# Optimization experiments

Measured on AMD Instinct MI355X. Metric: run time of the kernel, lower is better.

## Reference

```python
import jax, jax.numpy as jnp
import numpy as np

B, S, D, E = 8, 4096, 1024, 3
EPS = 1e-5


def setup_inputs() -> dict:
    key = jax.random.key(0)
    ks = jax.random.split(key, 4)
    s = 0.02  # init scale for weights
    return {
        "inputs": jax.random.normal(ks[0], (B, S, D), jnp.float32),
        "current_state": jnp.zeros((B, D), jnp.float32),
        "norm_w": jnp.ones((D,), jnp.float32),              # RMSNorm weight
        "router_w": jax.random.normal(ks[1], (D, E), jnp.float32) * s,
        "router_b": jnp.zeros((E,), jnp.float32),
        "w_gh": jax.random.normal(ks[2], (E, D, 2 * D), jnp.float32) * s,  # per-expert minGRU hidden+gate proj
        "w_out": jax.random.normal(ks[3], (E, D, D), jnp.float32) * s,     # per-expert proj_out
    }


def _rmsnorm(x, w, eps=EPS):
    return x * jax.lax.rsqrt(jnp.mean(x * x, axis=-1, keepdims=True) + eps) * w


def _g(x):
    # minGRU continuous activation g(x) = x + 0.5 for x >= 0 else sigmoid(x)
    return jnp.where(x >= 0, x + 0.5, jax.nn.sigmoid(x))


def reference(inputs, current_state, norm_w, router_w, router_b, w_gh, w_out):
    x = _rmsnorm(inputs, norm_w)                       # [B,S,D]
    # SMEAR: route per sample (mean-pooled features), soft-merge expert weights
    logits = jnp.mean(x, axis=1) @ router_w + router_b  # [B,E]
    probs = jax.nn.softmax(logits, axis=-1)             # [B,E]
    Wg = jnp.einsum('be,eij->bij', probs, w_gh)         # [B,D,2D] merged gate/hidden weights
    Wo = jnp.einsum('be,eij->bij', probs, w_out)        # [B,D,D]  merged output proj
    hg = jnp.einsum('bsi,bij->bsj', x, Wg)              # [B,S,2D]
    hid, gate = jnp.split(hg, 2, axis=-1)
    z = jax.nn.sigmoid(gate)                            # update gate
    a = 1.0 - z                                         # decay coefficient
    b = z * _g(hid)                                     # input term
    # fold initial state into first step: h_0 contribution
    b = b.at[:, 0].add(a[:, 0] * current_state)
    # linear recurrence h_t = a_t * h_{t-1} + b_t via associative scan over time
    def comb(c1, c2):
        a1, b1 = c1
        a2, b2 = c2
        return a1 * a2, a2 * b1 + b2
    _, h = jax.lax.associative_scan(comb, (a, b), axis=1)  # [B,S,D]
    new_state = h[:, -1]
    out = jnp.einsum('bsi,bij->bsj', h, Wo) + inputs       # proj_out + residual
    aux_loss = jnp.float32(0.0)
    return out, new_state, aux_loss
```

## Files before the change

kernel.cpp:

```cpp
#include <hip/hip_runtime.h>
#include <hip/hip_bf16.h>
#include <cstdint>
#include <cstddef>

using bf16 = __bf16;
typedef __bf16 bf16x8 __attribute__((ext_vector_type(8)));
typedef __bf16 bf16x4 __attribute__((ext_vector_type(4)));
typedef float  f32x4  __attribute__((ext_vector_type(4)));

#define DEV __device__ __forceinline__

DEV float sigmoidf_(float x) { return 1.0f / (1.0f + __expf(-x)); }

typedef __attribute__((address_space(1))) void as1_void;
typedef __attribute__((address_space(3))) void as3_void;

DEV void load16_lds(const void* g, void* l) {
  __builtin_amdgcn_global_load_lds((as1_void*)(void*)g, (as3_void*)l, 16, 0, 0);
}

__global__ __launch_bounds__(256) void k_rms_x(const float* __restrict__ inp,
                                               const float* __restrict__ nw,
                                               bf16* __restrict__ x) {
  const int row = blockIdx.x;
  const int t = threadIdx.x;
  const float* r = inp + (size_t)row * 1024 + t * 4;
  f32x4 v = *(const f32x4*)r;
  float ss = v[0]*v[0] + v[1]*v[1] + v[2]*v[2] + v[3]*v[3];
  __shared__ float red[4];
  for (int off = 32; off; off >>= 1) ss += __shfl_down(ss, off);
  if ((t & 63) == 0) red[t >> 6] = ss;
  __syncthreads();
  float tot = red[0] + red[1] + red[2] + red[3];
  float sc = rsqrtf(tot * (1.0f / 1024.0f) + 1e-5f);
  f32x4 w = *(const f32x4*)(nw + t * 4);
  bf16x4 o;
  o[0] = (bf16)(v[0] * sc * w[0]); o[1] = (bf16)(v[1] * sc * w[1]);
  o[2] = (bf16)(v[2] * sc * w[2]); o[3] = (bf16)(v[3] * sc * w[3]);
  *(bf16x4*)(x + (size_t)row * 1024 + t * 4) = o;
}

__global__ __launch_bounds__(256) void k_colsum(const bf16* __restrict__ x,
                                                float* __restrict__ part) {
  const int b = blockIdx.y, c = blockIdx.x;
  const int d = threadIdx.x * 4;
  f32x4 s = {0.f, 0.f, 0.f, 0.f};
  const bf16* base = x + ((size_t)b * 4096 + (size_t)c * 128) * 1024 + d;
  for (int i = 0; i < 128; ++i) {
    bf16x4 v = *(const bf16x4*)(base + (size_t)i * 1024);
    s[0] += (float)v[0]; s[1] += (float)v[1];
    s[2] += (float)v[2]; s[3] += (float)v[3];
  }
  *(f32x4*)(part + ((size_t)(b * 32 + c)) * 1024 + d) = s;
}

__global__ __launch_bounds__(256) void k_router(const float* __restrict__ part,
                                                const float* __restrict__ rw,
                                                const float* __restrict__ rb,
                                                float* __restrict__ probs,
                                                float* __restrict__ aux) {
  const int b = blockIdx.x;
  const int t = threadIdx.x;
  __shared__ float red[4];
  __shared__ float lg[3];
  f32x4 cs = {0.f, 0.f, 0.f, 0.f};
  #pragma unroll 8
  for (int c = 0; c < 32; ++c)
    cs += *(const f32x4*)(part + ((size_t)(b * 32 + c)) * 1024 + t * 4);
  for (int e = 0; e < 3; ++e) {
    float dot = cs[0] * rw[(t*4+0)*3+e] + cs[1] * rw[(t*4+1)*3+e]
              + cs[2] * rw[(t*4+2)*3+e] + cs[3] * rw[(t*4+3)*3+e];
    for (int off = 32; off; off >>= 1) dot += __shfl_down(dot, off);
    if ((t & 63) == 0) red[t >> 6] = dot;
    __syncthreads();
    if (t == 0) lg[e] = (red[0]+red[1]+red[2]+red[3]) * (1.0f/4096.0f) + rb[e];
    __syncthreads();
  }
  if (t == 0) {
    float m = fmaxf(lg[0], fmaxf(lg[1], lg[2]));
    float p0 = __expf(lg[0]-m), p1 = __expf(lg[1]-m), p2 = __expf(lg[2]-m);
    float inv = 1.0f / (p0 + p1 + p2);
    probs[b*3+0] = p0*inv; probs[b*3+1] = p1*inv; probs[b*3+2] = p2*inv;
    if (b == 0) *aux = 0.0f;
  }
}

__global__ __launch_bounds__(256) void k_mixT(const float* __restrict__ W,
                                              const float* __restrict__ probs,
                                              bf16* __restrict__ out,
                                              int Ncols) {
  const int b = blockIdx.z;
  const int i0 = blockIdx.y * 64;
  const int j0 = blockIdx.x * 64;
  const float p0 = probs[b*3+0], p1 = probs[b*3+1], p2 = probs[b*3+2];
  __shared__ float tile[64][68];
  const int t = threadIdx.x;
  const int jl = (t & 15) * 4;
  const size_t estr = (size_t)1024 * Ncols;
  for (int ii = 0; ii < 4; ++ii) {
    int il = (t >> 4) + ii * 16;
    const float* src = W + (size_t)(i0 + il) * Ncols + (j0 + jl);
    f32x4 v0 = *(const f32x4*)(src);
    f32x4 v1 = *(const f32x4*)(src + estr);
    f32x4 v2 = *(const f32x4*)(src + 2 * estr);
    f32x4 v = p0 * v0 + p1 * v1 + p2 * v2;
    tile[il][jl+0] = v[0]; tile[il][jl+1] = v[1];
    tile[il][jl+2] = v[2]; tile[il][jl+3] = v[3];
  }
  __syncthreads();
  bf16* ob = out + (size_t)b * Ncols * 1024;
  const int il2 = (t & 15) * 4;
  for (int jj = 0; jj < 4; ++jj) {
    int jl2 = (t >> 4) + jj * 16;
    bf16x4 o;
    o[0] = (bf16)tile[il2+0][jl2]; o[1] = (bf16)tile[il2+1][jl2];
    o[2] = (bf16)tile[il2+2][jl2]; o[3] = (bf16)tile[il2+3][jl2];
    *(bf16x4*)(ob + (size_t)(j0 + jl2) * 1024 + (i0 + il2)) = o;
  }
}

template<int EPI>
__global__ __launch_bounds__(512, 1) void k_gemm256(const bf16* __restrict__ A,
                                                    const bf16* __restrict__ Bt,
                                                    const float* __restrict__ addend,
                                                    float* __restrict__ Cout,
                                                    bf16* __restrict__ pa,
                                                    bf16* __restrict__ pb,
                                                    int M, int N, int K) {
  const int bz = blockIdx.z;
  const int nx = gridDim.x;
  const int nwg = nx * gridDim.y;
  const int orig = blockIdx.y * nx + blockIdx.x;
  const int swz = (orig & 7) * (nwg >> 3) + (orig >> 3);
  const int tm = swz / nx, tn = swz % nx;

  __shared__ __align__(16) char smem[131072];
  const int tid = threadIdx.x;
  const int lane = tid & 63, w = tid >> 6;
  const int l15 = lane & 15, quad = lane >> 4;
  const int wm = (w >> 2) * 128;
  const int wn = (w & 3) * 64;

  const bf16* Ab  = A  + (size_t)bz * M * K;
  const bf16* Btb = Bt + (size_t)bz * N * K;

  const int row0 = tid >> 3,          kc0 = (tid & 7) ^ (row0 & 7);
  const int row1 = (512 + tid) >> 3,  kc1 = (tid & 7) ^ (row1 & 7);

  auto browf = [&](int c) -> int {
    if constexpr (EPI == 0) {
      return tn * 128 + ((c >> 6) * 32) + (c & 31) + (((c & 63) >= 32) ? 1024 : 0);
    } else {
      return tn * 256 + c;
    }
  };
  const bf16* aS0_0 = Ab + (size_t)(tm*256 +       row0) * K + kc0 * 8;
  const bf16* aS0_1 = Ab + (size_t)(tm*256 +       row1) * K + kc1 * 8;
  const bf16* aS1_0 = Ab + (size_t)(tm*256 + 128 + row0) * K + kc0 * 8;
  const bf16* aS1_1 = Ab + (size_t)(tm*256 + 128 + row1) * K + kc1 * 8;
  const bf16* bS0_0 = Btb + (size_t)browf(row0)       * K + kc0 * 8;
  const bf16* bS0_1 = Btb + (size_t)browf(row1)       * K + kc1 * 8;
  const bf16* bS1_0 = Btb + (size_t)browf(128 + row0) * K + kc0 * 8;
  const bf16* bS1_1 = Btb + (size_t)browf(128 + row1) * K + kc1 * 8;

  const int ld0 = tid * 16;
  const int ld1 = 8192 + tid * 16;
  auto stage = [&](int buf, int u) {
    load16_lds(aS0_0 + u*64, smem + buf*32768 + ld0);
    load16_lds(aS0_1 + u*64, smem + buf*32768 + ld1);
    load16_lds(aS1_0 + u*64, smem + buf*32768 + 16384 + ld0);
    load16_lds(aS1_1 + u*64, smem + buf*32768 + 16384 + ld1);
    load16_lds(bS0_0 + u*64, smem + 65536 + buf*32768 + ld0);
    load16_lds(bS0_1 + u*64, smem + 65536 + buf*32768 + ld1);
    load16_lds(bS1_0 + u*64, smem + 65536 + buf*32768 + 16384 + ld0);
    load16_lds(bS1_1 + u*64, smem + 65536 + buf*32768 + 16384 + ld1);
  };

  f32x4 acc[8][4] = {};
  bf16x8 a[4][2], b0[2][2], b1[2][2];

  auto ldA = [&](int buf, int mq) {
    const bf16* base = (const bf16*)(smem + buf*32768);
    #pragma unroll
    for (int mi = 0; mi < 4; ++mi) {
      const int m = wm + mq*64 + mi*16 + l15;
      #pragma unroll
      for (int ks = 0; ks < 2; ++ks) {
        const int kc = ks*4 + quad;
        a[mi][ks] = *(const bf16x8*)(base + (size_t)(m*8 + (kc ^ (m & 7))) * 8);
      }
    }
  };
  auto ldB = [&](int buf, int nq, bf16x8 (&bb)[2][2]) {
    const bf16* base = (const bf16*)(smem + 65536 + buf*32768);
    #pragma unroll
    for (int ni = 0; ni < 2; ++ni) {
      const int n = wn + nq*32 + ni*16 + l15;
      #pragma unroll
      for (int ks = 0; ks < 2; ++ks) {
        const int kc = ks*4 + quad;
        bb[ni][ks] = *(const bf16x8*)(base + (size_t)(n*8 + (kc ^ (n & 7))) * 8);
      }
    }
  };

#define MMAC(MQ, NQ, BB)                                                        \
  _Pragma("unroll")                                                             \
  for (int mi = 0; mi < 4; ++mi) {                                              \
    _Pragma("unroll")                                                           \
    for (int ni = 0; ni < 2; ++ni) {                                            \
      f32x4 c_ = acc[(MQ)*4 + mi][(NQ)*2 + ni];                                 \
      c_ = __builtin_amdgcn_mfma_f32_16x16x32_bf16(a[mi][0], BB[ni][0], c_, 0, 0, 0); \
      c_ = __builtin_amdgcn_mfma_f32_16x16x32_bf16(a[mi][1], BB[ni][1], c_, 0, 0, 0); \
      acc[(MQ)*4 + mi][(NQ)*2 + ni] = c_;                                       \
    }                                                                           \
  }

  const int NT = K >> 6;

  stage(0, 0);
  __syncthreads();

  for (int t = 0; t < NT; ++t) {
    const int buf = t & 1;
    if (t + 1 < NT) stage(buf ^ 1, t + 1);
    ldA(buf, 0);
    ldB(buf, 0, b0);
    MMAC(0, 0, b0);
    ldB(buf, 1, b1);
    MMAC(0, 1, b1);
    ldA(buf, 1);
    MMAC(1, 1, b1);
    MMAC(1, 0, b0);
    __syncthreads();
  }

  if constexpr (EPI == 0) {
    bf16* Aab = pa + (size_t)bz * M * 1024;
    bf16* Bab = pb + (size_t)bz * M * 1024;
    const int jb = tn * 128 + (w & 3) * 32;
    const int rb = tm * 256 + wm;
    #pragma unroll
    for (int mi = 0; mi < 8; ++mi)
      #pragma unroll
      for (int ni = 0; ni < 2; ++ni)
        #pragma unroll
        for (int r = 0; r < 4; ++r) {
          const int srow = rb + mi * 16 + quad * 4 + r;
          float hid = acc[mi][ni][r];
          float gt  = acc[mi][ni + 2][r];
          float z = sigmoidf_(gt);
          float av = 1.0f - z;
          float gv = (hid >= 0.0f) ? (hid + 0.5f) : sigmoidf_(hid);
          float bv = z * gv;
          size_t oidx = (size_t)srow * 1024 + jb + ni * 16 + l15;
          Aab[oidx] = (bf16)av;
          Bab[oidx] = (bf16)bv;
        }
  } else {
    float* sC = (float*)smem;
    const int ST = 260;
    float* C = Cout + (size_t)bz * M * N;
    const float* Ain = addend + (size_t)bz * M * N;
    #pragma unroll
    for (int p = 0; p < 8; ++p) {
      if ((w >> 2) == (p >> 2)) {
        const int mi0 = (p & 3) * 2;
        #pragma unroll
        for (int mm = 0; mm < 2; ++mm)
          #pragma unroll
          for (int nt_ = 0; nt_ < 4; ++nt_)
            #pragma unroll
            for (int r = 0; r < 4; ++r) {
              const int rl = mm * 16 + quad * 4 + r;
              sC[rl * ST + (w & 3) * 64 + nt_ * 16 + l15] = acc[mi0 + mm][nt_][r];
            }
      }
      __syncthreads();
      #pragma unroll
      for (int i = 0; i < 4; ++i) {
        const int v = i * 512 + tid;
        const int rl = v >> 6, c4 = (v & 63) * 4;
        const int grow = tm * 256 + p * 32 + rl;
        const int gcol = tn * 256 + c4;
        f32x4 cv = *(f32x4*)(sC + rl * ST + c4);
        f32x4 ad = *(const f32x4*)(Ain + (size_t)grow * N + gcol);
        *(f32x4*)(C + (size_t)grow * N + gcol) = cv + ad;
      }
      __syncthreads();
    }
  }
#undef MMAC
}

__global__ __launch_bounds__(256) void k_scan1(const bf16* __restrict__ Aab,
                                               const bf16* __restrict__ Bab,
                                               float* __restrict__ cA,
                                               float* __restrict__ cB) {
  const int b = blockIdx.y, c = blockIdx.x;
  const int d = threadIdx.x * 4;
  f32x4 A = {1.f, 1.f, 1.f, 1.f}, Bv = {0.f, 0.f, 0.f, 0.f};
  const size_t base = ((size_t)(b * 4096 + c * 64)) * 1024 + d;
  #pragma unroll 4
  for (int i = 0; i < 64; ++i) {
    bf16x4 av = *(const bf16x4*)(Aab + base + (size_t)i * 1024);
    bf16x4 bv = *(const bf16x4*)(Bab + base + (size_t)i * 1024);
    #pragma unroll
    for (int j = 0; j < 4; ++j) {
      float a = (float)av[j], bb = (float)bv[j];
      A[j] *= a; Bv[j] = a * Bv[j] + bb;
    }
  }
  *(f32x4*)(cA + ((size_t)(b * 64 + c)) * 1024 + d) = A;
  *(f32x4*)(cB + ((size_t)(b * 64 + c)) * 1024 + d) = Bv;
}

__global__ __launch_bounds__(256) void k_scan2(const float* __restrict__ cA,
                                               const float* __restrict__ cB,
                                               const float* __restrict__ state,
                                               float* __restrict__ hin,
                                               float* __restrict__ ns) {
  const int gid = blockIdx.x * 256 + threadIdx.x;
  const int b = gid >> 10, d = gid & 1023;
  float h = state[gid];
  for (int c0 = 0; c0 < 64; c0 += 8) {
    float ar[8], br[8];
    #pragma unroll
    for (int i = 0; i < 8; ++i) {
      size_t idx = (((size_t)(b * 64 + c0 + i)) << 10) + d;
      ar[i] = cA[idx]; br[i] = cB[idx];
    }
    #pragma unroll
    for (int i = 0; i < 8; ++i) {
      size_t idx = (((size_t)(b * 64 + c0 + i)) << 10) + d;
      hin[idx] = h;
      h = ar[i] * h + br[i];
    }
  }
  ns[gid] = h;
}

__global__ __launch_bounds__(256) void k_scan3(const bf16* __restrict__ Aab,
                                               const bf16* __restrict__ Bab,
                                               const float* __restrict__ hin,
                                               bf16* __restrict__ hq) {
  const int b = blockIdx.y, c = blockIdx.x;
  const int d = threadIdx.x * 4;
  f32x4 h = *(const f32x4*)(hin + ((size_t)(b * 64 + c)) * 1024 + d);
  const size_t base = ((size_t)(b * 4096 + c * 64)) * 1024 + d;
  bf16* ob = hq + base;
  #pragma unroll 4
  for (int i = 0; i < 64; ++i) {
    bf16x4 av = *(const bf16x4*)(Aab + base + (size_t)i * 1024);
    bf16x4 bv = *(const bf16x4*)(Bab + base + (size_t)i * 1024);
    bf16x4 o;
    #pragma unroll
    for (int j = 0; j < 4; ++j) {
      h[j] = (float)av[j] * h[j] + (float)bv[j];
      o[j] = (bf16)h[j];
    }
    *(bf16x4*)(ob + (size_t)i * 1024) = o;
  }
}

extern "C" void kernel_launch(void* const* d_in, const int* in_sizes, int n_in,
                              void* d_out, int out_size, void* d_ws, size_t ws_size,
                              hipStream_t stream) {
  const float* inputs   = (const float*)d_in[0];
  const float* state    = (const float*)d_in[1];
  const float* norm_w   = (const float*)d_in[2];
  const float* router_w = (const float*)d_in[3];
  const float* router_b = (const float*)d_in[4];
  const float* w_gh     = (const float*)d_in[5];
  const float* w_out    = (const float*)d_in[6];

  float* out = (float*)d_out;
  float* new_state = out + (size_t)8 * 4096 * 1024;
  float* aux = new_state + 8 * 1024;

  char* ws = (char*)d_ws;
  size_t off = 0;
  auto alloc = [&](size_t bytes) {
    char* p = ws + off;
    off = (off + bytes + 255) & ~(size_t)255;
    return p;
  };
  bf16*  x    = (bf16*)alloc((size_t)8 * 4096 * 1024 * 2);
  bf16*  a_ar = (bf16*)alloc((size_t)8 * 4096 * 1024 * 2);
  bf16*  b_ar = (bf16*)alloc((size_t)8 * 4096 * 1024 * 2);
  bf16*  hq   = (bf16*)alloc((size_t)8 * 4096 * 1024 * 2);
  bf16*  WgT  = (bf16*)alloc((size_t)8 * 2048 * 1024 * 2);
  bf16*  WoT  = (bf16*)alloc((size_t)8 * 1024 * 1024 * 2);
  float* part = (float*)alloc((size_t)8 * 32 * 1024 * 4);
  float* probs = (float*)alloc(256);
  float* cA   = (float*)alloc((size_t)8 * 64 * 1024 * 4);
  float* cB   = (float*)alloc((size_t)8 * 64 * 1024 * 4);
  float* hin  = (float*)alloc((size_t)8 * 64 * 1024 * 4);
  (void)in_sizes; (void)n_in; (void)out_size; (void)ws_size;

  k_rms_x <<<32768, 256, 0, stream>>>(inputs, norm_w, x);
  k_colsum<<<dim3(32, 8), 256, 0, stream>>>(x, part);
  k_router<<<8, 256, 0, stream>>>(part, router_w, router_b, probs, aux);
  k_mixT  <<<dim3(32, 16, 8), 256, 0, stream>>>(w_gh, probs, WgT, 2048);
  k_mixT  <<<dim3(16, 16, 8), 256, 0, stream>>>(w_out, probs, WoT, 1024);
  k_gemm256<0><<<dim3(8, 16, 8), 512, 0, stream>>>(x, WgT, nullptr, nullptr,
                                                   a_ar, b_ar, 4096, 2048, 1024);
  k_scan1 <<<dim3(64, 8), 256, 0, stream>>>(a_ar, b_ar, cA, cB);
  k_scan2 <<<32, 256, 0, stream>>>(cA, cB, state, hin, new_state);
  k_scan3 <<<dim3(64, 8), 256, 0, stream>>>(a_ar, b_ar, hin, hq);
  k_gemm256<1><<<dim3(4, 16, 8), 512, 0, stream>>>(hq, WoT, inputs, out,
                                                   nullptr, nullptr, 4096, 1024, 1024);
}
```

Before: 580.1 us.

## Switch GEMM mainloop to 4-slot BK=32 pipeline with explicit vmcnt waits

Replaces the double-buffered BK=64 GEMM mainloop with a four-slot ring of BK=32 tiles kept three stages ahead. Each wait uses a fine-grained vmcnt count plus a raw s_barrier instead of a full __syncthreads, with a new paired-row swizzled LDS layout and precomputed fragment offsets. The aim is to hide global-to-LDS load latency better and cut sync cost. In exchange there are twice as many barriers per K, and the hand-counted vmcnt values and the slot reuse must be exactly right to avoid races.

```diff
diff --git a/kernel.cpp b/kernel.cpp
--- a/kernel.cpp
+++ b/kernel.cpp
@@ -18,6 +18,9 @@
 DEV void load16_lds(const void* g, void* l) {
   __builtin_amdgcn_global_load_lds((as1_void*)(void*)g, (as3_void*)l, 16, 0, 0);
 }
+
+#define SBAR()   __builtin_amdgcn_s_barrier()
+#define SCHED0() __builtin_amdgcn_sched_barrier(0)
 
 __global__ __launch_bounds__(256) void k_rms_x(const float* __restrict__ inp,
                                                const float* __restrict__ nw,
@@ -144,9 +147,6 @@
   const bf16* Ab  = A  + (size_t)bz * M * K;
   const bf16* Btb = Bt + (size_t)bz * N * K;
 
-  const int row0 = tid >> 3,          kc0 = (tid & 7) ^ (row0 & 7);
-  const int row1 = (512 + tid) >> 3,  kc1 = (tid & 7) ^ (row1 & 7);
-
   auto browf = [&](int c) -> int {
     if constexpr (EPI == 0) {
       return tn * 128 + ((c >> 6) * 32) + (c & 31) + (((c & 63) >= 32) ? 1024 : 0);
@@ -154,86 +154,76 @@
       return tn * 256 + c;
     }
   };
-  const bf16* aS0_0 = Ab + (size_t)(tm*256 +       row0) * K + kc0 * 8;
-  const bf16* aS0_1 = Ab + (size_t)(tm*256 +       row1) * K + kc1 * 8;
-  const bf16* aS1_0 = Ab + (size_t)(tm*256 + 128 + row0) * K + kc0 * 8;
-  const bf16* aS1_1 = Ab + (size_t)(tm*256 + 128 + row1) * K + kc1 * 8;
-  const bf16* bS0_0 = Btb + (size_t)browf(row0)       * K + kc0 * 8;
-  const bf16* bS0_1 = Btb + (size_t)browf(row1)       * K + kc1 * 8;
-  const bf16* bS1_0 = Btb + (size_t)browf(128 + row0) * K + kc0 * 8;
-  const bf16* bS1_1 = Btb + (size_t)browf(128 + row1) * K + kc1 * 8;
-
-  const int ld0 = tid * 16;
-  const int ld1 = 8192 + tid * 16;
-  auto stage = [&](int buf, int u) {
-    load16_lds(aS0_0 + u*64, smem + buf*32768 + ld0);
-    load16_lds(aS0_1 + u*64, smem + buf*32768 + ld1);
-    load16_lds(aS1_0 + u*64, smem + buf*32768 + 16384 + ld0);
-    load16_lds(aS1_1 + u*64, smem + buf*32768 + 16384 + ld1);
-    load16_lds(bS0_0 + u*64, smem + 65536 + buf*32768 + ld0);
-    load16_lds(bS0_1 + u*64, smem + 65536 + buf*32768 + ld1);
-    load16_lds(bS1_0 + u*64, smem + 65536 + buf*32768 + 16384 + ld0);
-    load16_lds(bS1_1 + u*64, smem + 65536 + buf*32768 + 16384 + ld1);
+
+  const int s7  = tid & 7;
+  const int r2a = tid >> 3;
+  const int g8v = s7 ^ (r2a & 7);
+  const int par = g8v >> 2;
+  const int gk  = g8v & 3;
+  const int rl0 = 2 * r2a + par;
+  const int rl1 = 128 + rl0;
+
+  const bf16* aSrc0 = Ab + (size_t)(tm*256 + rl0) * K + gk * 8;
+  const bf16* aSrc1 = Ab + (size_t)(tm*256 + rl1) * K + gk * 8;
+  const bf16* bSrc0 = Btb + (size_t)browf(rl0) * K + gk * 8;
+  const bf16* bSrc1 = Btb + (size_t)browf(rl1) * K + gk * 8;
+
+  auto stage = [&](int slot, int u) {
+    char* base = smem + slot * 32768;
+    load16_lds(aSrc0 + u*32, base + tid*16);
+    load16_lds(aSrc1 + u*32, base + 8192 + tid*16);
+    load16_lds(bSrc0 + u*32, base + 16384 + tid*16);
+    load16_lds(bSrc1 + u*32, base + 24576 + tid*16);
   };
 
+  int offA[8], offB[4];
+  #pragma unroll
+  for (int f = 0; f < 8; ++f) {
+    const int m = wm + (f >> 2) * 64 + (f & 3) * 16 + l15;
+    const int r2 = m >> 1;
+    offA[f] = r2 * 128 + (((((m & 1) << 2) | quad)) ^ (r2 & 7)) * 16;
+  }
+  #pragma unroll
+  for (int f = 0; f < 4; ++f) {
+    const int n = wn + (f >> 1) * 32 + (f & 1) * 16 + l15;
+    const int r2 = n >> 1;
+    offB[f] = r2 * 128 + (((((n & 1) << 2) | quad)) ^ (r2 & 7)) * 16;
+  }
+
   f32x4 acc[8][4] = {};
-  bf16x8 a[4][2], b0[2][2], b1[2][2];
-
-  auto ldA = [&](int buf, int mq) {
-    const bf16* base = (const bf16*)(smem + buf*32768);
-    #pragma unroll
-    for (int mi = 0; mi < 4; ++mi) {
-      const int m = wm + mq*64 + mi*16 + l15;
+  bf16x8 a[8], b[4];
+
+  const int NT = K >> 5;
+
+  stage(0, 0); stage(1, 1); stage(2, 2);
+  SCHED0();
+  asm volatile("s_waitcnt vmcnt(8)" ::: "memory");
+  SCHED0(); SBAR(); SCHED0();
+
+  for (int t = 0; t < NT; ++t) {
+    const int slot = t & 3;
+    if (t + 3 < NT) stage((t + 3) & 3, t + 3);
+    const char* ba = smem + slot * 32768;
+    const char* bbp = ba + 16384;
+    #pragma unroll
+    for (int f = 0; f < 8; ++f) a[f] = *(const bf16x8*)(ba + offA[f]);
+    #pragma unroll
+    for (int f = 0; f < 4; ++f) b[f] = *(const bf16x8*)(bbp + offB[f]);
+    #pragma unroll
+    for (int f = 0; f < 8; ++f)
       #pragma unroll
-      for (int ks = 0; ks < 2; ++ks) {
-        const int kc = ks*4 + quad;
-        a[mi][ks] = *(const bf16x8*)(base + (size_t)(m*8 + (kc ^ (m & 7))) * 8);
-      }
-    }
-  };
-  auto ldB = [&](int buf, int nq, bf16x8 (&bb)[2][2]) {
-    const bf16* base = (const bf16*)(smem + 65536 + buf*32768);
-    #pragma unroll
-    for (int ni = 0; ni < 2; ++ni) {
-      const int n = wn + nq*32 + ni*16 + l15;
-      #pragma unroll
-      for (int ks = 0; ks < 2; ++ks) {
-        const int kc = ks*4 + quad;
-        bb[ni][ks] = *(const bf16x8*)(base + (size_t)(n*8 + (kc ^ (n & 7))) * 8);
-      }
-    }
-  };
-
-#define MMAC(MQ, NQ, BB)                                                        \
-  _Pragma("unroll")                                                             \
-  for (int mi = 0; mi < 4; ++mi) {                                              \
-    _Pragma("unroll")                                                           \
-    for (int ni = 0; ni < 2; ++ni) {                                            \
-      f32x4 c_ = acc[(MQ)*4 + mi][(NQ)*2 + ni];                                 \
-      c_ = __builtin_amdgcn_mfma_f32_16x16x32_bf16(a[mi][0], BB[ni][0], c_, 0, 0, 0); \
-      c_ = __builtin_amdgcn_mfma_f32_16x16x32_bf16(a[mi][1], BB[ni][1], c_, 0, 0, 0); \
-      acc[(MQ)*4 + mi][(NQ)*2 + ni] = c_;                                       \
-    }                                                                           \
-  }
-
-  const int NT = K >> 6;
-
-  stage(0, 0);
+      for (int g = 0; g < 4; ++g)
+        acc[f][g] = __builtin_amdgcn_mfma_f32_16x16x32_bf16(a[f], b[g], acc[f][g], 0, 0, 0);
+    if (t + 1 < NT) {
+      SCHED0();
+      const int rem = NT - 2 - t;
+      if (rem >= 2)      { asm volatile("s_waitcnt vmcnt(8)" ::: "memory"); }
+      else if (rem == 1) { asm volatile("s_waitcnt vmcnt(4)" ::: "memory"); }
+      else               { asm volatile("s_waitcnt vmcnt(0)" ::: "memory"); }
+      SCHED0(); SBAR(); SCHED0();
+    }
+  }
   __syncthreads();
-
-  for (int t = 0; t < NT; ++t) {
-    const int buf = t & 1;
-    if (t + 1 < NT) stage(buf ^ 1, t + 1);
-    ldA(buf, 0);
-    ldB(buf, 0, b0);
-    MMAC(0, 0, b0);
-    ldB(buf, 1, b1);
-    MMAC(0, 1, b1);
-    ldA(buf, 1);
-    MMAC(1, 1, b1);
-    MMAC(1, 0, b0);
-    __syncthreads();
-  }
 
   if constexpr (EPI == 0) {
     bf16* Aab = pa + (size_t)bz * M * 1024;
@@ -290,7 +280,6 @@
       __syncthreads();
     }
   }
-#undef MMAC
 }
 
 __global__ __launch_bounds__(256) void k_scan1(const bf16* __restrict__ Aab,
```

Result: slower. 598.4 us (+3.1%).

## Restructure GEMM main loop into fine-grained half-tile prefetch pipeline with barriers and priorities

Applied to the files above, without the earlier changes.

Replaces the simple double-buffered GEMM loop with a schedule that splits each stage into A/B halves and issues global-to-LDS loads two iterations ahead, interleaved between MFMA quarter blocks. It uses explicit s_barrier, sched_barrier, manual vmcnt/lgkmcnt waits and s_setprio around MFMA clusters, with LDS offsets precomputed into registers. The aim is to hide global load latency and LDS reads behind matrix math. It adds more barriers per iteration and relies on hand-tuned wait counts, so the correctness of the buffer reuse timing is delicate.

```diff
diff --git a/kernel.cpp b/kernel.cpp
--- a/kernel.cpp
+++ b/kernel.cpp
@@ -18,6 +18,9 @@
 DEV void load16_lds(const void* g, void* l) {
   __builtin_amdgcn_global_load_lds((as1_void*)(void*)g, (as3_void*)l, 16, 0, 0);
 }
+
+#define SBAR()   __builtin_amdgcn_s_barrier()
+#define SCHED0() __builtin_amdgcn_sched_barrier(0)
 
 __global__ __launch_bounds__(256) void k_rms_x(const float* __restrict__ inp,
                                                const float* __restrict__ nw,
@@ -144,8 +147,8 @@
   const bf16* Ab  = A  + (size_t)bz * M * K;
   const bf16* Btb = Bt + (size_t)bz * N * K;
 
-  const int row0 = tid >> 3,          kc0 = (tid & 7) ^ (row0 & 7);
-  const int row1 = (512 + tid) >> 3,  kc1 = (tid & 7) ^ (row1 & 7);
+  const int rowh0 = tid >> 3,          kch0 = (tid & 7) ^ (rowh0 & 7);
+  const int rowh1 = (512 + tid) >> 3,  kch1 = (tid & 7) ^ (rowh1 & 7);
 
   auto browf = [&](int c) -> int {
     if constexpr (EPI == 0) {
@@ -154,86 +157,128 @@
       return tn * 256 + c;
     }
   };
-  const bf16* aS0_0 = Ab + (size_t)(tm*256 +       row0) * K + kc0 * 8;
-  const bf16* aS0_1 = Ab + (size_t)(tm*256 +       row1) * K + kc1 * 8;
-  const bf16* aS1_0 = Ab + (size_t)(tm*256 + 128 + row0) * K + kc0 * 8;
-  const bf16* aS1_1 = Ab + (size_t)(tm*256 + 128 + row1) * K + kc1 * 8;
-  const bf16* bS0_0 = Btb + (size_t)browf(row0)       * K + kc0 * 8;
-  const bf16* bS0_1 = Btb + (size_t)browf(row1)       * K + kc1 * 8;
-  const bf16* bS1_0 = Btb + (size_t)browf(128 + row0) * K + kc0 * 8;
-  const bf16* bS1_1 = Btb + (size_t)browf(128 + row1) * K + kc1 * 8;
-
-  const int ld0 = tid * 16;
-  const int ld1 = 8192 + tid * 16;
-  auto stage = [&](int buf, int u) {
-    load16_lds(aS0_0 + u*64, smem + buf*32768 + ld0);
-    load16_lds(aS0_1 + u*64, smem + buf*32768 + ld1);
-    load16_lds(aS1_0 + u*64, smem + buf*32768 + 16384 + ld0);
-    load16_lds(aS1_1 + u*64, smem + buf*32768 + 16384 + ld1);
-    load16_lds(bS0_0 + u*64, smem + 65536 + buf*32768 + ld0);
-    load16_lds(bS0_1 + u*64, smem + 65536 + buf*32768 + ld1);
-    load16_lds(bS1_0 + u*64, smem + 65536 + buf*32768 + 16384 + ld0);
-    load16_lds(bS1_1 + u*64, smem + 65536 + buf*32768 + 16384 + ld1);
+  const bf16* aS0_0 = Ab + (size_t)(tm*256 +       rowh0) * K + kch0 * 8;
+  const bf16* aS0_1 = Ab + (size_t)(tm*256 +       rowh1) * K + kch1 * 8;
+  const bf16* aS1_0 = Ab + (size_t)(tm*256 + 128 + rowh0) * K + kch0 * 8;
+  const bf16* aS1_1 = Ab + (size_t)(tm*256 + 128 + rowh1) * K + kch1 * 8;
+  const bf16* bS0_0 = Btb + (size_t)browf(rowh0)       * K + kch0 * 8;
+  const bf16* bS0_1 = Btb + (size_t)browf(rowh1)       * K + kch1 * 8;
+  const bf16* bS1_0 = Btb + (size_t)browf(128 + rowh0) * K + kch0 * 8;
+  const bf16* bS1_1 = Btb + (size_t)browf(128 + rowh1) * K + kch1 * 8;
+
+  auto stA = [&](int d, int h, int u) {
+    char* base = smem + (size_t)((d << 1) + h) * 16384;
+    load16_lds((h ? aS1_0 : aS0_0) + u * 64, base + tid * 16);
+    load16_lds((h ? aS1_1 : aS0_1) + u * 64, base + 8192 + tid * 16);
   };
-
-  f32x4 acc[8][4] = {};
-  bf16x8 a[4][2], b0[2][2], b1[2][2];
-
-  auto ldA = [&](int buf, int mq) {
-    const bf16* base = (const bf16*)(smem + buf*32768);
-    #pragma unroll
-    for (int mi = 0; mi < 4; ++mi) {
-      const int m = wm + mq*64 + mi*16 + l15;
+  auto stB = [&](int d, int h, int u) {
+    char* base = smem + 65536 + (size_t)((d << 1) + h) * 16384;
+    load16_lds((h ? bS1_0 : bS0_0) + u * 64, base + tid * 16);
+    load16_lds((h ? bS1_1 : bS0_1) + u * 64, base + 8192 + tid * 16);
+  };
+
+  const int ha = wm >> 7, hb = wn >> 7;
+  const int wnl = wn & 127;
+  int offA[2][4][2], offB[2][2][2];
+  #pragma unroll
+  for (int mq = 0; mq < 2; ++mq)
+    #pragma unroll
+    for (int mi = 0; mi < 4; ++mi)
       #pragma unroll
       for (int ks = 0; ks < 2; ++ks) {
-        const int kc = ks*4 + quad;
-        a[mi][ks] = *(const bf16x8*)(base + (size_t)(m*8 + (kc ^ (m & 7))) * 8);
+        const int mr = mq * 64 + mi * 16 + l15;
+        offA[mq][mi][ks] = mr * 128 + (((ks * 4 + quad)) ^ (mr & 7)) * 16;
       }
-    }
-  };
-  auto ldB = [&](int buf, int nq, bf16x8 (&bb)[2][2]) {
-    const bf16* base = (const bf16*)(smem + 65536 + buf*32768);
-    #pragma unroll
-    for (int ni = 0; ni < 2; ++ni) {
-      const int n = wn + nq*32 + ni*16 + l15;
+  #pragma unroll
+  for (int nq = 0; nq < 2; ++nq)
+    #pragma unroll
+    for (int ni = 0; ni < 2; ++ni)
       #pragma unroll
       for (int ks = 0; ks < 2; ++ks) {
-        const int kc = ks*4 + quad;
-        bb[ni][ks] = *(const bf16x8*)(base + (size_t)(n*8 + (kc ^ (n & 7))) * 8);
+        const int nr = wnl + nq * 32 + ni * 16 + l15;
+        offB[nq][ni][ks] = nr * 128 + (((ks * 4 + quad)) ^ (nr & 7)) * 16;
       }
-    }
-  };
-
-#define MMAC(MQ, NQ, BB)                                                        \
+
+  f32x4 acc[8][4] = {};
+  bf16x8 a0[4][2], a1[4][2], b0[2][2], b1[2][2];
+
+#define MMAC(MQ, NQ, AA, BB)                                                    \
   _Pragma("unroll")                                                             \
   for (int mi = 0; mi < 4; ++mi) {                                              \
     _Pragma("unroll")                                                           \
     for (int ni = 0; ni < 2; ++ni) {                                            \
       f32x4 c_ = acc[(MQ)*4 + mi][(NQ)*2 + ni];                                 \
-      c_ = __builtin_amdgcn_mfma_f32_16x16x32_bf16(a[mi][0], BB[ni][0], c_, 0, 0, 0); \
-      c_ = __builtin_amdgcn_mfma_f32_16x16x32_bf16(a[mi][1], BB[ni][1], c_, 0, 0, 0); \
+      c_ = __builtin_amdgcn_mfma_f32_16x16x32_bf16(AA[mi][0], BB[ni][0], c_, 0, 0, 0); \
+      c_ = __builtin_amdgcn_mfma_f32_16x16x32_bf16(AA[mi][1], BB[ni][1], c_, 0, 0, 0); \
       acc[(MQ)*4 + mi][(NQ)*2 + ni] = c_;                                       \
     }                                                                           \
   }
 
   const int NT = K >> 6;
 
-  stage(0, 0);
+  stB(0, 0, 0); stB(0, 1, 0); stA(0, 0, 0); stA(0, 1, 0);
+  stB(1, 0, 1); stB(1, 1, 1); stA(1, 0, 1);
+  SCHED0();
+  asm volatile("s_waitcnt vmcnt(6)" ::: "memory");
+  SCHED0(); SBAR(); SCHED0();
+
+  for (int t = 0; t < NT; ++t) {
+    const int d = t & 1, nd = d ^ 1;
+    const char* Abase = smem + (size_t)((d << 1) + ha) * 16384;
+    const char* Bbase = smem + 65536 + (size_t)((d << 1) + hb) * 16384;
+    #pragma unroll
+    for (int mi = 0; mi < 4; ++mi) {
+      a0[mi][0] = *(const bf16x8*)(Abase + offA[0][mi][0]);
+      a0[mi][1] = *(const bf16x8*)(Abase + offA[0][mi][1]);
+    }
+    #pragma unroll
+    for (int ni = 0; ni < 2; ++ni) {
+      b0[ni][0] = *(const bf16x8*)(Bbase + offB[0][ni][0]);
+      b0[ni][1] = *(const bf16x8*)(Bbase + offB[0][ni][1]);
+      b1[ni][0] = *(const bf16x8*)(Bbase + offB[1][ni][0]);
+      b1[ni][1] = *(const bf16x8*)(Bbase + offB[1][ni][1]);
+    }
+    if (t + 1 < NT) stA(nd, 1, t + 1);
+    SCHED0(); SBAR(); SCHED0();
+    asm volatile("s_waitcnt lgkmcnt(0)" ::: "memory");
+    SCHED0();
+    __builtin_amdgcn_s_setprio(1);
+    MMAC(0, 0, a0, b0);
+    __builtin_amdgcn_s_setprio(0);
+    SCHED0(); SBAR(); SCHED0();
+    #pragma unroll
+    for (int mi = 0; mi < 4; ++mi) {
+      a1[mi][0] = *(const bf16x8*)(Abase + offA[1][mi][0]);
+      a1[mi][1] = *(const bf16x8*)(Abase + offA[1][mi][1]);
+    }
+    if (t + 2 < NT) stB(d, 0, t + 2);
+    SCHED0(); SBAR(); SCHED0();
+    asm volatile("s_waitcnt lgkmcnt(0)" ::: "memory");
+    SCHED0();
+    __builtin_amdgcn_s_setprio(1);
+    MMAC(0, 1, a0, b1);
+    __builtin_amdgcn_s_setprio(0);
+    SCHED0(); SBAR(); SCHED0();
+    if (t + 2 < NT) stB(d, 1, t + 2);
+    SCHED0(); SBAR(); SCHED0();
+    __builtin_amdgcn_s_setprio(1);
+    MMAC(1, 1, a1, b1);
+    __builtin_amdgcn_s_setprio(0);
+    SCHED0(); SBAR(); SCHED0();
+    if (t + 2 < NT) stA(d, 0, t + 2);
+    SCHED0(); SBAR(); SCHED0();
+    __builtin_amdgcn_s_setprio(1);
+    MMAC(1, 0, a1, b0);
+    __builtin_amdgcn_s_setprio(0);
+    SCHED0();
+    if (t + 2 < NT) {
+      asm volatile("s_waitcnt vmcnt(6)" ::: "memory");
+    } else if (t + 1 < NT) {
+      asm volatile("s_waitcnt vmcnt(0)" ::: "memory");
+    }
+    SCHED0(); SBAR(); SCHED0();
+  }
   __syncthreads();
-
-  for (int t = 0; t < NT; ++t) {
-    const int buf = t & 1;
-    if (t + 1 < NT) stage(buf ^ 1, t + 1);
-    ldA(buf, 0);
-    ldB(buf, 0, b0);
-    MMAC(0, 0, b0);
-    ldB(buf, 1, b1);
-    MMAC(0, 1, b1);
-    ldA(buf, 1);
-    MMAC(1, 1, b1);
-    MMAC(1, 0, b0);
-    __syncthreads();
-  }
 
   if constexpr (EPI == 0) {
     bf16* Aab = pa + (size_t)bz * M * 1024;
```

Result: slower. 601.1 us (+3.6%).

## Fuse RMSNorm with column-sum partials and merge both weight-mixing launches

Applied to the files above, without the earlier changes.

RMSNorm and the per-sample column sum now run in one kernel: each wave normalizes 16 rows, writes bf16 x, and accumulates fp32 column partials that are reduced through LDS. This avoids re-reading x from global memory and drops a launch. The router now sums 64 partials instead of 32. The two weight-mix launches become a single grid that branches on blockIdx.x, which removes another launch. The fused kernel runs only 512 blocks, far fewer than the previous 32768, which may leave memory bandwidth underused. Column sums are also taken on the fp32 values before bf16 rounding, which slightly changes numerics.

```diff
diff --git a/kernel.cpp b/kernel.cpp
--- a/kernel.cpp
+++ b/kernel.cpp
@@ -19,39 +19,54 @@
   __builtin_amdgcn_global_load_lds((as1_void*)(void*)g, (as3_void*)l, 16, 0, 0);
 }
 
-__global__ __launch_bounds__(256) void k_rms_x(const float* __restrict__ inp,
-                                               const float* __restrict__ nw,
-                                               bf16* __restrict__ x) {
-  const int row = blockIdx.x;
+__global__ __launch_bounds__(256) void k_rms_colsum(const float* __restrict__ inp,
+                                                    const float* __restrict__ nw,
+                                                    bf16* __restrict__ x,
+                                                    float* __restrict__ part) {
+  const int b = blockIdx.y, c = blockIdx.x;
+  const int w = threadIdx.x >> 6, lane = threadIdx.x & 63;
+  __shared__ float sC[4][1024];
+  f32x4 wv[4];
+  #pragma unroll
+  for (int k = 0; k < 4; ++k) wv[k] = *(const f32x4*)(nw + lane * 16 + k * 4);
+  f32x4 accp[4] = {};
+  const size_t rowbase = (size_t)b * 4096 + (size_t)c * 64;
+  #pragma unroll 4
+  for (int i = 0; i < 16; ++i) {
+    const int row = w * 16 + i;
+    const float* r = inp + (rowbase + row) * 1024 + lane * 16;
+    f32x4 v[4];
+    #pragma unroll
+    for (int k = 0; k < 4; ++k) v[k] = *(const f32x4*)(r + k * 4);
+    float ss = 0.f;
+    #pragma unroll
+    for (int k = 0; k < 4; ++k)
+      ss += v[k][0]*v[k][0] + v[k][1]*v[k][1] + v[k][2]*v[k][2] + v[k][3]*v[k][3];
+    #pragma unroll
+    for (int off = 32; off; off >>= 1) ss += __shfl_xor(ss, off);
+    const float sc = rsqrtf(ss * (1.0f / 1024.0f) + 1e-5f);
+    bf16* xo = x + (rowbase + row) * 1024 + lane * 16;
+    #pragma unroll
+    for (int k = 0; k < 4; ++k) {
+      f32x4 nv;
+      nv[0] = v[k][0] * sc * wv[k][0]; nv[1] = v[k][1] * sc * wv[k][1];
+      nv[2] = v[k][2] * sc * wv[k][2]; nv[3] = v[k][3] * sc * wv[k][3];
+      accp[k][0] += nv[0]; accp[k][1] += nv[1];
+      accp[k][2] += nv[2]; accp[k][3] += nv[3];
+      bf16x4 o;
+      o[0] = (bf16)nv[0]; o[1] = (bf16)nv[1]; o[2] = (bf16)nv[2]; o[3] = (bf16)nv[3];
+      *(bf16x4*)(xo + k * 4) = o;
+    }
+  }
+  #pragma unroll
+  for (int k = 0; k < 4; ++k) *(f32x4*)(&sC[w][lane * 16 + k * 4]) = accp[k];
+  __syncthreads();
   const int t = threadIdx.x;
-  const float* r = inp + (size_t)row * 1024 + t * 4;
-  f32x4 v = *(const f32x4*)r;
-  float ss = v[0]*v[0] + v[1]*v[1] + v[2]*v[2] + v[3]*v[3];
-  __shared__ float red[4];
-  for (int off = 32; off; off >>= 1) ss += __shfl_down(ss, off);
-  if ((t & 63) == 0) red[t >> 6] = ss;
-  __syncthreads();
-  float tot = red[0] + red[1] + red[2] + red[3];
-  float sc = rsqrtf(tot * (1.0f / 1024.0f) + 1e-5f);
-  f32x4 w = *(const f32x4*)(nw + t * 4);
-  bf16x4 o;
-  o[0] = (bf16)(v[0] * sc * w[0]); o[1] = (bf16)(v[1] * sc * w[1]);
-  o[2] = (bf16)(v[2] * sc * w[2]); o[3] = (bf16)(v[3] * sc * w[3]);
-  *(bf16x4*)(x + (size_t)row * 1024 + t * 4) = o;
-}
-
-__global__ __launch_bounds__(256) void k_colsum(const bf16* __restrict__ x,
-                                                float* __restrict__ part) {
-  const int b = blockIdx.y, c = blockIdx.x;
-  const int d = threadIdx.x * 4;
-  f32x4 s = {0.f, 0.f, 0.f, 0.f};
-  const bf16* base = x + ((size_t)b * 4096 + (size_t)c * 128) * 1024 + d;
-  for (int i = 0; i < 128; ++i) {
-    bf16x4 v = *(const bf16x4*)(base + (size_t)i * 1024);
-    s[0] += (float)v[0]; s[1] += (float)v[1];
-    s[2] += (float)v[2]; s[3] += (float)v[3];
-  }
-  *(f32x4*)(part + ((size_t)(b * 32 + c)) * 1024 + d) = s;
+  f32x4 s = *(const f32x4*)(&sC[0][t * 4]);
+  s += *(const f32x4*)(&sC[1][t * 4]);
+  s += *(const f32x4*)(&sC[2][t * 4]);
+  s += *(const f32x4*)(&sC[3][t * 4]);
+  *(f32x4*)(part + ((size_t)(b * 64 + c)) * 1024 + t * 4) = s;
 }
 
 __global__ __launch_bounds__(256) void k_router(const float* __restrict__ part,
@@ -65,8 +80,8 @@
   __shared__ float lg[3];
   f32x4 cs = {0.f, 0.f, 0.f, 0.f};
   #pragma unroll 8
-  for (int c = 0; c < 32; ++c)
-    cs += *(const f32x4*)(part + ((size_t)(b * 32 + c)) * 1024 + t * 4);
+  for (int c = 0; c < 64; ++c)
+    cs += *(const f32x4*)(part + ((size_t)(b * 64 + c)) * 1024 + t * 4);
   for (int e = 0; e < 3; ++e) {
     float dot = cs[0] * rw[(t*4+0)*3+e] + cs[1] * rw[(t*4+1)*3+e]
               + cs[2] * rw[(t*4+2)*3+e] + cs[3] * rw[(t*4+3)*3+e];
@@ -85,13 +100,17 @@
   }
 }
 
-__global__ __launch_bounds__(256) void k_mixT(const float* __restrict__ W,
-                                              const float* __restrict__ probs,
-                                              bf16* __restrict__ out,
-                                              int Ncols) {
+__global__ __launch_bounds__(256) void k_mixT2(const float* __restrict__ Wg,
+                                               const float* __restrict__ Wo,
+                                               const float* __restrict__ probs,
+                                               bf16* __restrict__ og,
+                                               bf16* __restrict__ oo) {
+  const int xb = blockIdx.x;
+  const float* W; bf16* out; int Ncols; int j0;
+  if (xb < 32) { W = Wg; out = og; Ncols = 2048; j0 = xb * 64; }
+  else         { W = Wo; out = oo; Ncols = 1024; j0 = (xb - 32) * 64; }
   const int b = blockIdx.z;
   const int i0 = blockIdx.y * 64;
-  const int j0 = blockIdx.x * 64;
   const float p0 = probs[b*3+0], p1 = probs[b*3+1], p2 = probs[b*3+2];
   __shared__ float tile[64][68];
   const int t = threadIdx.x;
@@ -391,18 +410,16 @@
   bf16*  hq   = (bf16*)alloc((size_t)8 * 4096 * 1024 * 2);
   bf16*  WgT  = (bf16*)alloc((size_t)8 * 2048 * 1024 * 2);
   bf16*  WoT  = (bf16*)alloc((size_t)8 * 1024 * 1024 * 2);
-  float* part = (float*)alloc((size_t)8 * 32 * 1024 * 4);
+  float* part = (float*)alloc((size_t)8 * 64 * 1024 * 4);
   float* probs = (float*)alloc(256);
   float* cA   = (float*)alloc((size_t)8 * 64 * 1024 * 4);
   float* cB   = (float*)alloc((size_t)8 * 64 * 1024 * 4);
   float* hin  = (float*)alloc((size_t)8 * 64 * 1024 * 4);
   (void)in_sizes; (void)n_in; (void)out_size; (void)ws_size;
 
-  k_rms_x <<<32768, 256, 0, stream>>>(inputs, norm_w, x);
-  k_colsum<<<dim3(32, 8), 256, 0, stream>>>(x, part);
-  k_router<<<8, 256, 0, stream>>>(part, router_w, router_b, probs, aux);
-  k_mixT  <<<dim3(32, 16, 8), 256, 0, stream>>>(w_gh, probs, WgT, 2048);
-  k_mixT  <<<dim3(16, 16, 8), 256, 0, stream>>>(w_out, probs, WoT, 1024);
+  k_rms_colsum<<<dim3(64, 8), 256, 0, stream>>>(inputs, norm_w, x, part);
+  k_router <<<8, 256, 0, stream>>>(part, router_w, router_b, probs, aux);
+  k_mixT2  <<<dim3(48, 16, 8), 256, 0, stream>>>(w_gh, w_out, probs, WgT, WoT);
   k_gemm256<0><<<dim3(8, 16, 8), 512, 0, stream>>>(x, WgT, nullptr, nullptr,
                                                    a_ar, b_ar, 4096, 2048, 1024);
   k_scan1 <<<dim3(64, 8), 256, 0, stream>>>(a_ar, b_ar, cA, cB);
```

Result: slower. 629.8 us (+8.6%).
